# Performance work log

Hardware: AMD Instinct MI355X
Metric: run time of the kernel (lower is better)

Reference implementation:

```python
import jax, jax.numpy as jnp
import numpy as np

# task -> non-background class ids, padded with -1 to fixed width 3
NBG = np.array([[0, 1, 2], [0, 3, 4], [0, 5, 6], [0, 7, 8],
                [0, 9, -1], [0, 10, -1], [0, 11, -1]], dtype=np.int32)
NEG = -1e9      # pad logit (finite stand-in for -inf, grad-safe)
SMOOTH = 1e-5
NUM_CLASSES = 12


def setup_inputs() -> dict:
    key = jax.random.key(0)
    k1, k2, k3 = jax.random.split(key, 3)
    B, C, D, H, W = 4, 12, 32, 128, 128
    inputs = jax.random.normal(k1, (B, C, D, H, W), dtype=jnp.float32)
    task_id = jax.random.randint(k2, (B,), 0, 7, dtype=jnp.int32)
    # build targets consistent with each sample's task: labels in task_nbg[task]
    raw = jax.random.randint(k3, (B, D, H, W), 0, 3, dtype=jnp.int32)
    nbg = jnp.asarray(NBG)
    ids = nbg[task_id]                                   # [B,3]
    valid_max = jnp.where(ids[:, 2] < 0, 1, 2)           # 2-class tasks: raw in {0,1}
    raw = jnp.minimum(raw, valid_max[:, None, None, None])
    targets = jnp.take_along_axis(ids, raw.reshape(B, -1), axis=1).reshape(B, D, H, W)
    return {"inputs": inputs, "targets": targets, "task_id": task_id}


def reference(inputs, targets, task_id):
    B = inputs.shape[0]
    probs = jax.nn.softmax(inputs, axis=1)               # [B,12,D,H,W]
    nbg = jnp.asarray(NBG)
    ids = nbg[task_id]                                   # [B,3]
    mask = (ids >= 0)                                    # [B,3]
    idsc = jnp.maximum(ids, 0)
    mask5 = mask[:, :, None, None, None]
    gathered = jnp.take_along_axis(probs, idsc[:, :, None, None, None], axis=1)  # [B,3,D,H,W]
    score = jnp.where(mask5, gathered, 0.0)

    # --- remapped marginal targets: labels > 0 shifted by delta ---
    t = task_id.astype(jnp.int32)
    delta = jnp.where(t <= 4, -2 * t, -t - 4)
    tm = jnp.where(targets > 0, targets + delta[:, None, None, None], targets)   # in {0,1,2}

    # --- marginal CE: log_softmax over gathered probs (note: probs, not logits, matching torch F.cross_entropy on softmaxed inputs) ---
    logits = jnp.where(mask5, gathered, NEG)
    logp = jax.nn.log_softmax(logits, axis=1)
    nll = -jnp.take_along_axis(logp, tm[:, None], axis=1)[:, 0]                  # [B,D,H,W]
    loss_marg_ce = nll.mean(axis=(1, 2, 3)).sum() / B

    # --- marginal dice (padded classes contribute exactly 0) ---
    tgt = ((targets[:, None] == idsc[:, :, None, None, None]) & mask5).astype(probs.dtype)
    inter = jnp.sum(score * tgt, axis=(2, 3, 4))
    y_sum = jnp.sum(tgt, axis=(2, 3, 4))                 # tgt is binary: tgt*tgt == tgt
    z_sum = jnp.sum(score * score, axis=(2, 3, 4))
    dice = (2 * inter + SMOOTH) / (z_sum + y_sum + SMOOTH)
    loss_marg_dice = (1.0 - dice).sum() / B

    # --- exclusion: target_e = 1 - onehot(targets, 0..11), class 0 zeroed ---
    cls = jnp.arange(NUM_CLASSES, dtype=targets.dtype)[None, :, None, None, None]
    onehot = (targets[:, None] == cls).astype(probs.dtype)
    te = 1.0 - onehot
    te = te.at[:, 0].set(0.0)
    inter_e = jnp.sum(probs * te, axis=(2, 3, 4))
    y_e = jnp.sum(te, axis=(2, 3, 4))
    z_e = jnp.sum(probs * probs, axis=(2, 3, 4))
    dice_e = (2 * inter_e + SMOOTH) / (z_e + y_e + SMOOTH)
    loss_exc_dice = dice_e.sum() / B                     # inv=True: sum of dice scores

    loss_exc_ce = (jnp.log1p(probs) * te).mean(axis=(2, 3, 4)).sum() / B

    return (loss_marg_dice, loss_marg_ce, loss_exc_dice, loss_exc_ce)
```

## Files before the change

kernel.cpp:

```cpp
#include <hip/hip_runtime.h>


#define S4 131072
#define BLOCKS_PER_B 256
#define THREADS 256
#define NVOX 524288.0f
#define SMOOTH 1e-5f
#define L2E 1.4426950408889634f
#define LN2 0.6931471805599453f

#define WRED(v) { v += __shfl_down(v,32); v += __shfl_down(v,16); \
                  v += __shfl_down(v,8);  v += __shfl_down(v,4);  \
                  v += __shfl_down(v,2);  v += __shfl_down(v,1); }

__global__ void zero_acc(float* __restrict__ acc) {
  acc[blockIdx.x * 256 + threadIdx.x] = 0.f;
}

#define TAIL(CM) {                                                             \
  const int tv = tg.CM;                                                        \
  const bool t0 = (tv == 0), t1 = (tv == id1), t2 = (tv == id2);               \
  c1f += t1 ? 1.f : 0.f;  c2f += t2 ? 1.f : 0.f;                               \
  p0S += t0 ? g0.CM : 0.f; p1S += t1 ? g1.CM : 0.f; p2S += t2 ? g2.CM : 0.f;   \
  const float pt = t1 ? g1.CM : (t2 ? g2.CM : 0.f);                            \
  cesE2 += __builtin_amdgcn_logf(prod.CM * __builtin_amdgcn_rcpf(1.f + pt));   \
  const float s3 = __builtin_amdgcn_exp2f(g0.CM * L2E)                         \
                 + __builtin_amdgcn_exp2f(g1.CM * L2E)                         \
                 + __builtin_amdgcn_exp2f(g2.CM * L2E);                        \
  const float gt = t0 ? g0.CM : (t1 ? g1.CM : g2.CM);                          \
  ces2 += __builtin_amdgcn_logf(s3) - gt * L2E;                                \
}

#define COMPUTE(E, GE1, GE2, TG) {                                             \
  _Pragma("unroll")                                                            \
  for (int c = 0; c < 12; ++c) {                                               \
    E[c].x = __builtin_amdgcn_exp2f(E[c].x * L2E);                             \
    E[c].y = __builtin_amdgcn_exp2f(E[c].y * L2E);                             \
    E[c].z = __builtin_amdgcn_exp2f(E[c].z * L2E);                             \
    E[c].w = __builtin_amdgcn_exp2f(E[c].w * L2E);                             \
  }                                                                            \
  float4 es = E[0];                                                            \
  _Pragma("unroll")                                                            \
  for (int c = 1; c < 12; ++c) {                                               \
    es.x += E[c].x; es.y += E[c].y; es.z += E[c].z; es.w += E[c].w;            \
  }                                                                            \
  float4 r;                                                                    \
  r.x = __builtin_amdgcn_rcpf(es.x); r.y = __builtin_amdgcn_rcpf(es.y);        \
  r.z = __builtin_amdgcn_rcpf(es.z); r.w = __builtin_amdgcn_rcpf(es.w);        \
  float4 prod = make_float4(1.f, 1.f, 1.f, 1.f);                               \
  _Pragma("unroll")                                                            \
  for (int c = 0; c < 12; ++c) {                                               \
    float4 p;                                                                  \
    p.x = E[c].x * r.x; p.y = E[c].y * r.y;                                    \
    p.z = E[c].z * r.z; p.w = E[c].w * r.w;                                    \
    aZ[c] += (p.x*p.x + p.y*p.y) + (p.z*p.z + p.w*p.w);                        \
    aP[c] += (p.x + p.y) + (p.z + p.w);                                        \
    if (c > 0) {                                                               \
      prod.x = fmaf(prod.x, p.x, prod.x);                                      \
      prod.y = fmaf(prod.y, p.y, prod.y);                                      \
      prod.z = fmaf(prod.z, p.z, prod.z);                                      \
      prod.w = fmaf(prod.w, p.w, prod.w);                                      \
    }                                                                          \
  }                                                                            \
  float4 g0, g1, g2;                                                           \
  g0.x = E[0].x * r.x; g0.y = E[0].y * r.y;                                    \
  g0.z = E[0].z * r.z; g0.w = E[0].w * r.w;                                    \
  g1.x = __builtin_amdgcn_exp2f(GE1.x * L2E) * r.x;                            \
  g1.y = __builtin_amdgcn_exp2f(GE1.y * L2E) * r.y;                            \
  g1.z = __builtin_amdgcn_exp2f(GE1.z * L2E) * r.z;                            \
  g1.w = __builtin_amdgcn_exp2f(GE1.w * L2E) * r.w;                            \
  g2.x = v2 ? __builtin_amdgcn_exp2f(GE2.x * L2E) * r.x : -1e30f;              \
  g2.y = v2 ? __builtin_amdgcn_exp2f(GE2.y * L2E) * r.y : -1e30f;              \
  g2.z = v2 ? __builtin_amdgcn_exp2f(GE2.z * L2E) * r.z : -1e30f;              \
  g2.w = v2 ? __builtin_amdgcn_exp2f(GE2.w * L2E) * r.w : -1e30f;              \
  const int4 tg = TG;                                                          \
  TAIL(x); TAIL(y); TAIL(z); TAIL(w);                                          \
}

__global__ __launch_bounds__(THREADS, 2)
void marg_main(const float4* __restrict__ inp, const int4* __restrict__ tgtp,
               const int* __restrict__ task_id, float* __restrict__ acc) {
  const int b   = blockIdx.x / BLOCKS_PER_B;
  const int blk = blockIdx.x % BLOCKS_PER_B;
  const int t   = task_id[b];
  const int id1 = (t <= 4) ? 2*t + 1 : t + 5;
  const int id2 = (t <= 3) ? 2*t + 2 : -1;
  const bool v2 = (id2 >= 0);
  const int id2c = v2 ? id2 : 0;

  const float4* inB = inp  + (size_t)b * 12 * S4;
  const int4*   tgB = tgtp + (size_t)b * S4;

  float aZ[12], aP[12];
  #pragma unroll
  for (int c = 0; c < 12; ++c) { aZ[c] = 0.f; aP[c] = 0.f; }
  float ces2=0.f, cesE2=0.f, c1f=0.f, c2f=0.f, p0S=0.f, p1S=0.f, p2S=0.f;

  const int s0 = blk * (2 * THREADS) + (int)threadIdx.x;
  const int s1 = s0 + THREADS;

  float4 xa[12], xb[12];
  #pragma unroll
  for (int c = 0; c < 12; ++c) xa[c] = inB[(size_t)c * S4 + s0];
  float4 ga1 = inB[(size_t)id1 * S4 + s0];
  float4 ga2 = inB[(size_t)id2c * S4 + s0];
  const int4 ta = tgB[s0];
  #pragma unroll
  for (int c = 0; c < 12; ++c) xb[c] = inB[(size_t)c * S4 + s1];
  float4 gb1 = inB[(size_t)id1 * S4 + s1];
  float4 gb2 = inB[(size_t)id2c * S4 + s1];
  const int4 tb = tgB[s1];

  COMPUTE(xa, ga1, ga2, ta);
  COMPUTE(xb, gb1, gb2, tb);

  WRED(ces2); WRED(cesE2); WRED(c1f); WRED(c2f);
  WRED(p0S);  WRED(p1S);   WRED(p2S);
  #pragma unroll
  for (int c = 0; c < 12; ++c) { WRED(aZ[c]); WRED(aP[c]); }

  __shared__ float red[4][32];
  const int lane = threadIdx.x & 63;
  const int wv   = threadIdx.x >> 6;
  if (lane == 0) {
    float* rw = red[wv];
    #pragma unroll
    for (int c = 0; c < 12; ++c) { rw[c] = aZ[c]; rw[12 + c] = aP[c]; }
    rw[24] = ces2; rw[25] = cesE2; rw[26] = c1f; rw[27] = c2f;
    rw[28] = p0S;  rw[29] = p1S;   rw[30] = p2S; rw[31] = 0.f;
  }
  __syncthreads();
  if (threadIdx.x < 32) {
    const float sv = red[0][threadIdx.x] + red[1][threadIdx.x]
                   + red[2][threadIdx.x] + red[3][threadIdx.x];
    atomicAdd(acc + ((b * 32 + (int)threadIdx.x) << 4), sv);
  }
}

__global__ void finalize(const float* __restrict__ acc,
                         const int* __restrict__ task_id,
                         float* __restrict__ out) {
  if (threadIdx.x != 0) return;
  float lmd = 0.f, lmce = 0.f, led = 0.f, lece = 0.f;
  for (int b = 0; b < 4; ++b) {
    const int t   = task_id[b];
    const int id1 = (t <= 4) ? 2*t + 1 : t + 5;
    const int id2 = (t <= 3) ? 2*t + 2 : -1;
    #define A(v) acc[((b * 32 + (v))) << 4]

    lmce += A(24) * LN2 / NVOX;
    lece += A(25) * LN2 / NVOX;

    const float c1 = A(26), c2 = A(27);
    const float y0 = NVOX - c1 - c2;
    const float d0 = (2.f*A(28) + SMOOTH) / (A(0)   + y0 + SMOOTH);
    const float d1 = (2.f*A(29) + SMOOTH) / (A(id1) + c1 + SMOOTH);
    float d2 = 1.f;
    if (id2 >= 0)
      d2 = (2.f*A(30) + SMOOTH) / (A(id2) + c2 + SMOOTH);
    lmd += (1.f - d0) + (1.f - d1) + (1.f - d2);

    led += SMOOTH / (A(0) + SMOOTH);
    for (int c = 1; c < 12; ++c) {
      const float ptc  = (c == id1) ? A(29) : ((c == id2) ? A(30) : 0.f);
      const float cntc = (c == id1) ? c1    : ((c == id2) ? c2    : 0.f);
      const float inter = A(12 + c) - ptc;
      const float ye    = NVOX - cntc;
      led += (2.f*inter + SMOOTH) / (A(c) + ye + SMOOTH);
    }
    #undef A
  }
  out[0] = lmd  * 0.25f;
  out[1] = lmce * 0.25f;
  out[2] = led  * 0.25f;
  out[3] = lece * 0.25f;
}

extern "C" void kernel_launch(void* const* d_in, const int* in_sizes, int n_in,
                              void* d_out, int out_size, void* d_ws, size_t ws_size,
                              hipStream_t stream) {
  const float* inputs  = (const float*)d_in[0];
  const int*   targets = (const int*)d_in[1];
  const int*   task_id = (const int*)d_in[2];
  float* out = (float*)d_out;
  float* acc = (float*)d_ws;

  zero_acc<<<dim3(8), 256, 0, stream>>>(acc);
  marg_main<<<dim3(4 * BLOCKS_PER_B), THREADS, 0, stream>>>(
      (const float4*)inputs, (const int4*)targets, task_id, acc);
  finalize<<<1, 64, 0, stream>>>(acc, task_id, out);
}
```

Baseline: 181.8 us.

## Stream input tiles through double-buffered LDS with async global-to-LDS loads

The main kernel now uses fewer, smaller blocks, and each block loops over 8 tiles of voxel groups. Each tile's 12 class planes and its targets are staged into a double-buffered shared-memory buffer with global_load_lds, and the next tile is prefetched while the current one is computed. The id1/id2 gathered logits are read back from LDS rather than reloaded from global memory, which removes two redundant global loads per group. The aim is to overlap loads with compute and cut register pressure. In exchange there are fewer resident waves and less memory traffic in flight, plus a per-tile barrier, and correctness depends on the barrier also waiting for the async LDS loads to finish.

```diff
diff --git a/kernel.cpp b/kernel.cpp
--- a/kernel.cpp
+++ b/kernel.cpp
@@ -2,8 +2,10 @@
 
 
 #define S4 131072
-#define BLOCKS_PER_B 256
-#define THREADS 256
+#define BLOCKS_PER_B 128
+#define THREADS 128
+#define GROUPS 128
+#define NTILES 8
 #define NVOX 524288.0f
 #define SMOOTH 1e-5f
 #define L2E 1.4426950408889634f
@@ -15,6 +17,12 @@
 
 __global__ void zero_acc(float* __restrict__ acc) {
   acc[blockIdx.x * 256 + threadIdx.x] = 0.f;
+}
+
+__device__ __forceinline__ void gload_lds16(const float4* g, float4* ldsbase) {
+  __builtin_amdgcn_global_load_lds(
+      (const __attribute__((address_space(1))) void*)g,
+      (__attribute__((address_space(3))) void*)ldsbase, 16, 0, 0);
 }
 
 #define TAIL(CM) {                                                             \
@@ -31,18 +39,28 @@
   ces2 += __builtin_amdgcn_logf(s3) - gt * L2E;                                \
 }
 
-#define COMPUTE(E, GE1, GE2, TG) {                                             \
+#define STAGE(T, PB) {                                                         \
+  const int g = base + (T) * GROUPS + tid;                                     \
+  _Pragma("unroll")                                                            \
+  for (int c = 0; c < 12; ++c)                                                 \
+    gload_lds16(&inB[(size_t)c * S4 + g], &sbuf[PB][c][wv << 6]);              \
+  gload_lds16((const float4*)&tgB[g], (float4*)&stg[PB][wv << 6]);             \
+}
+
+#define COMPUTE(PB) {                                                          \
+  float4 xv[12];                                                               \
   _Pragma("unroll")                                                            \
   for (int c = 0; c < 12; ++c) {                                               \
-    E[c].x = __builtin_amdgcn_exp2f(E[c].x * L2E);                             \
-    E[c].y = __builtin_amdgcn_exp2f(E[c].y * L2E);                             \
-    E[c].z = __builtin_amdgcn_exp2f(E[c].z * L2E);                             \
-    E[c].w = __builtin_amdgcn_exp2f(E[c].w * L2E);                             \
+    const float4 v = sbuf[PB][c][tid];                                         \
+    xv[c].x = __builtin_amdgcn_exp2f(v.x * L2E);                               \
+    xv[c].y = __builtin_amdgcn_exp2f(v.y * L2E);                               \
+    xv[c].z = __builtin_amdgcn_exp2f(v.z * L2E);                               \
+    xv[c].w = __builtin_amdgcn_exp2f(v.w * L2E);                               \
   }                                                                            \
-  float4 es = E[0];                                                            \
+  float4 es = xv[0];                                                           \
   _Pragma("unroll")                                                            \
   for (int c = 1; c < 12; ++c) {                                               \
-    es.x += E[c].x; es.y += E[c].y; es.z += E[c].z; es.w += E[c].w;            \
+    es.x += xv[c].x; es.y += xv[c].y; es.z += xv[c].z; es.w += xv[c].w;        \
   }                                                                            \
   float4 r;                                                                    \
   r.x = __builtin_amdgcn_rcpf(es.x); r.y = __builtin_amdgcn_rcpf(es.y);        \
@@ -51,8 +69,8 @@
   _Pragma("unroll")                                                            \
   for (int c = 0; c < 12; ++c) {                                               \
     float4 p;                                                                  \
-    p.x = E[c].x * r.x; p.y = E[c].y * r.y;                                    \
-    p.z = E[c].z * r.z; p.w = E[c].w * r.w;                                    \
+    p.x = xv[c].x * r.x; p.y = xv[c].y * r.y;                                  \
+    p.z = xv[c].z * r.z; p.w = xv[c].w * r.w;                                  \
     aZ[c] += (p.x*p.x + p.y*p.y) + (p.z*p.z + p.w*p.w);                        \
     aP[c] += (p.x + p.y) + (p.z + p.w);                                        \
     if (c > 0) {                                                               \
@@ -62,66 +80,66 @@
       prod.w = fmaf(prod.w, p.w, prod.w);                                      \
     }                                                                          \
   }                                                                            \
+  const float4 v1  = sbuf[PB][id1][tid];                                       \
+  const float4 vv2 = sbuf[PB][id2c][tid];                                      \
   float4 g0, g1, g2;                                                           \
-  g0.x = E[0].x * r.x; g0.y = E[0].y * r.y;                                    \
-  g0.z = E[0].z * r.z; g0.w = E[0].w * r.w;                                    \
-  g1.x = __builtin_amdgcn_exp2f(GE1.x * L2E) * r.x;                            \
-  g1.y = __builtin_amdgcn_exp2f(GE1.y * L2E) * r.y;                            \
-  g1.z = __builtin_amdgcn_exp2f(GE1.z * L2E) * r.z;                            \
-  g1.w = __builtin_amdgcn_exp2f(GE1.w * L2E) * r.w;                            \
-  g2.x = v2 ? __builtin_amdgcn_exp2f(GE2.x * L2E) * r.x : -1e30f;              \
-  g2.y = v2 ? __builtin_amdgcn_exp2f(GE2.y * L2E) * r.y : -1e30f;              \
-  g2.z = v2 ? __builtin_amdgcn_exp2f(GE2.z * L2E) * r.z : -1e30f;              \
-  g2.w = v2 ? __builtin_amdgcn_exp2f(GE2.w * L2E) * r.w : -1e30f;              \
-  const int4 tg = TG;                                                          \
+  g0.x = xv[0].x * r.x; g0.y = xv[0].y * r.y;                                  \
+  g0.z = xv[0].z * r.z; g0.w = xv[0].w * r.w;                                  \
+  g1.x = __builtin_amdgcn_exp2f(v1.x * L2E) * r.x;                             \
+  g1.y = __builtin_amdgcn_exp2f(v1.y * L2E) * r.y;                             \
+  g1.z = __builtin_amdgcn_exp2f(v1.z * L2E) * r.z;                             \
+  g1.w = __builtin_amdgcn_exp2f(v1.w * L2E) * r.w;                             \
+  g2.x = v2 ? __builtin_amdgcn_exp2f(vv2.x * L2E) * r.x : -1e30f;              \
+  g2.y = v2 ? __builtin_amdgcn_exp2f(vv2.y * L2E) * r.y : -1e30f;              \
+  g2.z = v2 ? __builtin_amdgcn_exp2f(vv2.z * L2E) * r.z : -1e30f;              \
+  g2.w = v2 ? __builtin_amdgcn_exp2f(vv2.w * L2E) * r.w : -1e30f;              \
+  const int4 tg = stg[PB][tid];                                                \
   TAIL(x); TAIL(y); TAIL(z); TAIL(w);                                          \
 }
 
-__global__ __launch_bounds__(THREADS, 2)
+__global__ __launch_bounds__(THREADS, 1)
 void marg_main(const float4* __restrict__ inp, const int4* __restrict__ tgtp,
                const int* __restrict__ task_id, float* __restrict__ acc) {
-  const int b   = blockIdx.x / BLOCKS_PER_B;
-  const int blk = blockIdx.x % BLOCKS_PER_B;
-  const int t   = task_id[b];
-  const int id1 = (t <= 4) ? 2*t + 1 : t + 5;
-  const int id2 = (t <= 3) ? 2*t + 2 : -1;
-  const bool v2 = (id2 >= 0);
+  __shared__ float4 sbuf[2][12][GROUPS];
+  __shared__ int4   stg[2][GROUPS];
+  __shared__ float  red[2][32];
+
+  const int b    = blockIdx.x / BLOCKS_PER_B;
+  const int blk  = blockIdx.x % BLOCKS_PER_B;
+  const int tid  = threadIdx.x;
+  const int wv   = tid >> 6;
+  const int lane = tid & 63;
+  const int t    = task_id[b];
+  const int id1  = (t <= 4) ? 2*t + 1 : t + 5;
+  const int id2  = (t <= 3) ? 2*t + 2 : -1;
+  const bool v2  = (id2 >= 0);
   const int id2c = v2 ? id2 : 0;
 
   const float4* inB = inp  + (size_t)b * 12 * S4;
   const int4*   tgB = tgtp + (size_t)b * S4;
+  const int base = blk * (NTILES * GROUPS);
 
   float aZ[12], aP[12];
   #pragma unroll
   for (int c = 0; c < 12; ++c) { aZ[c] = 0.f; aP[c] = 0.f; }
   float ces2=0.f, cesE2=0.f, c1f=0.f, c2f=0.f, p0S=0.f, p1S=0.f, p2S=0.f;
 
-  const int s0 = blk * (2 * THREADS) + (int)threadIdx.x;
-  const int s1 = s0 + THREADS;
-
-  float4 xa[12], xb[12];
+  STAGE(0, 0);
+  __syncthreads();
+
   #pragma unroll
-  for (int c = 0; c < 12; ++c) xa[c] = inB[(size_t)c * S4 + s0];
-  float4 ga1 = inB[(size_t)id1 * S4 + s0];
-  float4 ga2 = inB[(size_t)id2c * S4 + s0];
-  const int4 ta = tgB[s0];
-  #pragma unroll
-  for (int c = 0; c < 12; ++c) xb[c] = inB[(size_t)c * S4 + s1];
-  float4 gb1 = inB[(size_t)id1 * S4 + s1];
-  float4 gb2 = inB[(size_t)id2c * S4 + s1];
-  const int4 tb = tgB[s1];
-
-  COMPUTE(xa, ga1, ga2, ta);
-  COMPUTE(xb, gb1, gb2, tb);
+  for (int tt = 0; tt < NTILES; ++tt) {
+    const int cur = tt & 1, nxt = cur ^ 1;
+    if (tt + 1 < NTILES) STAGE(tt + 1, nxt);
+    COMPUTE(cur);
+    __syncthreads();
+  }
 
   WRED(ces2); WRED(cesE2); WRED(c1f); WRED(c2f);
   WRED(p0S);  WRED(p1S);   WRED(p2S);
   #pragma unroll
   for (int c = 0; c < 12; ++c) { WRED(aZ[c]); WRED(aP[c]); }
 
-  __shared__ float red[4][32];
-  const int lane = threadIdx.x & 63;
-  const int wv   = threadIdx.x >> 6;
   if (lane == 0) {
     float* rw = red[wv];
     #pragma unroll
@@ -130,10 +148,9 @@
     rw[28] = p0S;  rw[29] = p1S;   rw[30] = p2S; rw[31] = 0.f;
   }
   __syncthreads();
-  if (threadIdx.x < 32) {
-    const float sv = red[0][threadIdx.x] + red[1][threadIdx.x]
-                   + red[2][threadIdx.x] + red[3][threadIdx.x];
-    atomicAdd(acc + ((b * 32 + (int)threadIdx.x) << 4), sv);
+  if (tid < 32) {
+    const float sv = red[0][tid] + red[1][tid];
+    atomicAdd(acc + ((b * 32 + tid) << 4), sv);
   }
 }
 
```

Result: slower. 201.9 us (+11.1%).
